# Optimization experiments

Measured on AMD Instinct MI355X. Metric: run time of the kernel, lower is better.

Reference implementation:

```python
import jax, jax.numpy as jnp
import numpy as np

B, L, S, M, N = 128, 3, 256, 256, 20000
NS, A, NL = 4, 5, 2
MAP_RANGE = 10.0
DELTA_VAR = 0.1
EPS = 1e-5


def _ln(x):
    mu = jnp.mean(x, -1, keepdims=True)
    var = jnp.var(x, -1, keepdims=True)
    return (x - mu) / jnp.sqrt(var + EPS)


def _cal_map_last(map_pts, anchor_last):
    # map_pts: [2, N], anchor_last: [B, 1, L] -> [B, M, 2]
    pos = anchor_last[:, 0, 0:2]
    d = map_pts[None, :, :] - pos[:, :, None]                    # [B,2,N]
    th = anchor_last[:, 0, -1]
    c, s = jnp.cos(th), jnp.sin(th)
    rot = jnp.stack([jnp.stack([c, s], -1), jnp.stack([-s, c], -1)], 1)  # [B,2,2]
    m = jnp.einsum('bij,bjn->bin', rot, d)                       # ego-frame points
    dis = jnp.sqrt(jnp.sum(m * m, axis=1, keepdims=True))        # [B,1,N]
    m = jnp.where(dis >= MAP_RANGE, 1e10, m)
    m = jnp.sort(m, axis=-1)                                     # per-coordinate sort (as in torch)
    m = jnp.where(m >= 1e9, 0.0, m)
    m = m[:, :, :M]                                              # torch F.pad negative pad == crop to map_num_max
    return jnp.transpose(m, (0, 2, 1))


def _forward(inp_start_point, map_pts, end_point, delta_limit_mean,
             W_enc_anchor, Wq, Wk, Wv, W_in, W_out, W_map1, W_map2,
             W_ih0, W_ih1, W_hh0, W_hh1, W_m1, W_m2, W_v1, W_v2):
    anchor = inp_start_point
    var_last = jnp.ones_like(anchor) * 0.01  # never updated, as in torch source
    pre_mean, pre_var, views = [], [], []
    scale = 1.0 / np.sqrt(S)                 # MHA 1 head -> head_dim = S
    bsz = anchor.shape[0]
    for step in range(NS):
        dm, dv = [anchor], [var_last]
        vt = [jnp.transpose(_cal_map_last(map_pts, anchor), (0, 2, 1))]
        h = jnp.ones((NL, bsz, S), anchor.dtype)
        c = jnp.ones((NL, bsz, S), anchor.dtype)
        for _ in range(A - 1):
            enc_a = _ln(jnp.concatenate([anchor, anchor - end_point, var_last], -1) @ W_enc_anchor[step].T)  # [B,1,S]
            ml = jax.lax.stop_gradient(_cal_map_last(map_pts, anchor))  # torch.no_grad in encode_last_map
            q = ml @ Wq[step].T
            k = ml @ Wk[step].T
            v = ml @ Wv[step].T
            wq, wk, wv = jnp.split(W_in[step], 3, axis=0)
            q2 = q @ wq.T
            k2 = k @ wk.T
            v2 = v @ wv.T
            attn = jax.nn.softmax(jnp.einsum('bqs,bks->bqk', q2, k2) * scale, axis=-1)
            o = jnp.einsum('bqk,bks->bqs', attn, v2) @ W_out[step].T    # [B,M,S]
            x = jax.nn.relu(jnp.transpose(o, (0, 2, 1)))                # [B,S,M]
            x = jax.nn.relu(x @ W_map1[step].T) @ W_map2[step].T        # [B,S,1]
            enc_m = _ln(jnp.transpose(x, (0, 2, 1)))                    # [B,1,S]
            xl = jnp.concatenate([enc_a, enc_m], -1)[:, 0, :]           # [B,2S], single LSTM timestep
            hs, cs = [], []
            for l, (Wih, Whh) in enumerate(((W_ih0[step], W_hh0[step]), (W_ih1[step], W_hh1[step]))):
                g = xl @ Wih.T + h[l] @ Whh.T
                i_g, f_g, g_g, o_g = jnp.split(g, 4, -1)               # torch gate order i,f,g,o
                cl = jax.nn.sigmoid(f_g) * c[l] + jax.nn.sigmoid(i_g) * jnp.tanh(g_g)
                hl = jax.nn.sigmoid(o_g) * jnp.tanh(cl)
                hs.append(hl)
                cs.append(cl)
                xl = hl
            h, c = jnp.stack(hs), jnp.stack(cs)
            mn = _ln(xl)[:, None, :]                                    # [B,1,S]
            mean = jnp.tanh(jax.nn.relu(jax.nn.relu(mn) @ W_m1[step].T) @ W_m2[step].T) * delta_limit_mean + anchor
            varr = jax.nn.sigmoid(jax.nn.relu(jax.nn.relu(mn) @ W_v1[step].T) @ W_v2[step].T) * DELTA_VAR
            dm.append(mean)
            dv.append(varr)
            anchor = mean
            vt.append(jnp.transpose(_cal_map_last(map_pts, anchor), (0, 2, 1)))
        pre_mean.append(jnp.concatenate(dm, 1)[:, None])    # [B,1,A,L]
        pre_var.append(jnp.concatenate(dv, 1)[:, None])
        views.append(jnp.stack(vt, 1)[:, None])             # [B,1,A,2,M]
    return (jnp.concatenate(pre_mean, 1), jnp.concatenate(pre_var, 1), jnp.concatenate(views, 1))


def setup_inputs() -> dict:
    key = jax.random.key(0)
    ks = jax.random.split(key, 20)

    def w(k, shape, fan):
        return jax.random.normal(k, shape, jnp.float32) / np.sqrt(fan)

    return {
        'inp_start_point': jax.random.normal(ks[0], (B, 1, L), jnp.float32) * 2.0,
        'map_pts': jax.random.uniform(ks[1], (2, N), jnp.float32, -50.0, 50.0),
        'end_point': jnp.array([5.0, 5.0, 0.0], jnp.float32),
        'delta_limit_mean': jnp.array([1.0, 1.0, 0.3], jnp.float32),
        'W_enc_anchor': w(ks[2], (NS, S, 3 * L), 3 * L),
        'Wq': w(ks[3], (NS, S, 2), 2),
        'Wk': w(ks[4], (NS, S, 2), 2),
        'Wv': w(ks[5], (NS, S, 2), 2),
        'W_in': w(ks[6], (NS, 3 * S, S), S),
        'W_out': w(ks[7], (NS, S, S), S),
        'W_map1': w(ks[8], (NS, S, M), M),
        'W_map2': w(ks[9], (NS, 1, S), S),
        'W_ih0': w(ks[10], (NS, 4 * S, 2 * S), 2 * S),
        'W_ih1': w(ks[11], (NS, 4 * S, S), S),
        'W_hh0': w(ks[12], (NS, 4 * S, S), S),
        'W_hh1': w(ks[13], (NS, 4 * S, S), S),
        'W_m1': w(ks[14], (NS, S, S), S),
        'W_m2': w(ks[15], (NS, L, S), S),
        'W_v1': w(ks[16], (NS, S, S), S),
        'W_v2': w(ks[17], (NS, L, S), S),
    }


def reference(inp_start_point, map_pts, end_point, delta_limit_mean,
              W_enc_anchor, Wq, Wk, Wv, W_in, W_out, W_map1, W_map2,
              W_ih0, W_ih1, W_hh0, W_hh1, W_m1, W_m2, W_v1, W_v2):
    return _forward(inp_start_point, map_pts, end_point, delta_limit_mean,
                    W_enc_anchor, Wq, Wk, Wv, W_in, W_out, W_map1, W_map2,
                    W_ih0, W_ih1, W_hh0, W_hh1, W_m1, W_m2, W_v1, W_v2)
```

## Files before the change

### kernel.cpp

```cpp
#include <hip/hip_runtime.h>

#define BB 128
#define NPTS 20000
#define NSTEP 4
#define NITER 4

#define OFF_ANCHOR 0
#define OFF_G      384
#define OFF_AO     400
#define OFF_U      2448
#define OFF_XL     67984
#define OFF_OUT    133520
#define OFF_H      166288
#define OFF_C      231824
#define OFF_GB     297360
#define OFF_RMN    428432
#define OFF_TM     461200
#define OFF_TV     493968

#define OUT_VAR   7680
#define OUT_VIEWS 15360

__device__ __forceinline__ float sigf(float x){ return 1.0f/(1.0f+expf(-x)); }

__device__ __forceinline__ float blockSum256(float v, float* buf){
    for (int off = 32; off > 0; off >>= 1) v += __shfl_down(v, off, 64);
    int tid = threadIdx.x;
    __syncthreads();
    if ((tid & 63) == 0) buf[tid >> 6] = v;
    __syncthreads();
    return (buf[0] + buf[1]) + (buf[2] + buf[3]);
}

__device__ __forceinline__ double blockSum256d(double v, double* buf){
    for (int off = 32; off > 0; off >>= 1) v += __shfl_down(v, off, 64);
    int tid = threadIdx.x;
    __syncthreads();
    if ((tid & 63) == 0) buf[tid >> 6] = v;
    __syncthreads();
    return (buf[0] + buf[1]) + (buf[2] + buf[3]);
}

__global__ __launch_bounds__(256) void k_init(const float* __restrict__ inp, float* __restrict__ ws)
{
    int i = blockIdx.x*256 + threadIdx.x;
    if (i < BB*3) ws[OFF_ANCHOR + i] = inp[i];
}

__global__ __launch_bounds__(256) void k_pre(const float* __restrict__ Wq, const float* __restrict__ Wk,
                                             const float* __restrict__ Wv, const float* __restrict__ Win,
                                             const float* __restrict__ Wout, float* __restrict__ ws)
{
    __shared__ float wql[512], wkl[512], wvl[512];
    __shared__ double avl[512];
    __shared__ double dbuf[4];
    int s = blockIdx.x, t = threadIdx.x;
    wql[t] = Wq[s*512 + t];   wql[256+t] = Wq[s*512 + 256 + t];
    wkl[t] = Wk[s*512 + t];   wkl[256+t] = Wk[s*512 + 256 + t];
    wvl[t] = Wv[s*512 + t];   wvl[256+t] = Wv[s*512 + 256 + t];
    __syncthreads();
    const float* wq = Win + s*196608 + t*256;
    const float* wk = wq + 65536;
    const float* wv = wq + 131072;
    double aq0=0,aq1=0,ak0=0,ak1=0,av0=0,av1=0;
    for (int j = 0; j < 256; j++){
        double a = wq[j], b = wk[j], c = wv[j];
        aq0 += a*(double)wql[j*2]; aq1 += a*(double)wql[j*2+1];
        ak0 += b*(double)wkl[j*2]; ak1 += b*(double)wkl[j*2+1];
        av0 += c*(double)wvl[j*2]; av1 += c*(double)wvl[j*2+1];
    }
    avl[t*2] = av0; avl[t*2+1] = av1;
    double g00 = blockSum256d(aq0*ak0, dbuf);
    double g01 = blockSum256d(aq0*ak1, dbuf);
    double g10 = blockSum256d(aq1*ak0, dbuf);
    double g11 = blockSum256d(aq1*ak1, dbuf);
    if (t == 0){
        ws[OFF_G + s*4+0] = (float)g00; ws[OFF_G + s*4+1] = (float)g01;
        ws[OFF_G + s*4+2] = (float)g10; ws[OFF_G + s*4+3] = (float)g11;
    }
    const float* wo = Wout + s*65536 + t*256;
    double o0 = 0.0, o1 = 0.0;
    for (int j = 0; j < 256; j++){
        double w = wo[j];
        o0 += w*avl[j*2]; o1 += w*avl[j*2+1];
    }
    ws[OFF_AO + s*512 + t*2]   = (float)o0;
    ws[OFF_AO + s*512 + t*2+1] = (float)o1;
}

__global__ __launch_bounds__(256) void k_step_init(float* __restrict__ ws, float* __restrict__ out, int s)
{
    int gid = blockIdx.x*256 + threadIdx.x;
    if (gid < 2*BB*256){ ws[OFF_H + gid] = 1.0f; ws[OFF_C + gid] = 1.0f; }
    if (gid < BB*3){
        int b = gid/3, j = gid - b*3;
        out[((b*NSTEP + s)*5 + 0)*3 + j] = ws[OFF_ANCHOR + gid];
        out[OUT_VAR + ((b*NSTEP + s)*5 + 0)*3 + j] = 0.01f;
    }
}

__global__ __launch_bounds__(256) void k_map(const float* __restrict__ mp, float* __restrict__ ws,
                                             float* __restrict__ out, int s, int t)
{
    __shared__ unsigned int histx[2048], histy[2048];
    __shared__ float vx[1024], vy[1024];
    __shared__ float candx[512], candy[512];
    __shared__ float sortx[256], sorty[256];
    __shared__ int scanb[256];
    __shared__ int shjx, shjy;
    __shared__ unsigned int cnt_in, cntx, cnty;
    int tid = threadIdx.x, b = blockIdx.x;
    float ax = ws[OFF_ANCHOR + b*3 + 0];
    float ay = ws[OFF_ANCHOR + b*3 + 1];
    float th = ws[OFF_ANCHOR + b*3 + 2];
    float cth = cosf(th), sth = sinf(th);
    for (int i = tid; i < 2048; i += 256){ histx[i] = 0u; histy[i] = 0u; }
    if (tid == 0){ cnt_in = 0u; cntx = 0u; cnty = 0u; }
    __syncthreads();
    for (int i = tid; i < NPTS; i += 256){
        float dx = mp[i] - ax, dy = mp[NPTS + i] - ay;
        float rx = cth*dx + sth*dy;
        float ry = cth*dy - sth*dx;
        float d  = sqrtf(rx*rx + ry*ry);
        if (d < 10.0f){
            unsigned p = atomicAdd(&cnt_in, 1u);
            if (p < 1024u){ vx[p] = rx; vy[p] = ry; }
            int bx = (int)((rx + 10.0f) * 102.4f); bx = min(max(bx, 0), 2047);
            int by = (int)((ry + 10.0f) * 102.4f); by = min(max(by, 0), 2047);
            atomicAdd(&histx[bx], 1u); atomicAdd(&histy[by], 1u);
        }
    }
    __syncthreads();
    int total = (int)min(cnt_in, 1024u);
    int K = min(256, total);
    {
        int part = 0;
        for (int k = 0; k < 8; k++) part += (int)histx[tid*8 + k];
        scanb[tid] = part; __syncthreads();
        for (int off = 1; off < 256; off <<= 1){
            int v = (tid >= off) ? scanb[tid - off] : 0; __syncthreads();
            scanb[tid] += v; __syncthreads();
        }
        int incl = scanb[tid], excl = incl - part;
        if (K > 0 && excl < K && incl >= K){
            int c = excl;
            for (int k = 0; k < 8; k++){ c += (int)histx[tid*8+k]; if (c >= K){ shjx = tid*8+k; break; } }
        }
        if (K == 0 && tid == 0) shjx = -1;
        __syncthreads();
    }
    {
        int part = 0;
        for (int k = 0; k < 8; k++) part += (int)histy[tid*8 + k];
        scanb[tid] = part; __syncthreads();
        for (int off = 1; off < 256; off <<= 1){
            int v = (tid >= off) ? scanb[tid - off] : 0; __syncthreads();
            scanb[tid] += v; __syncthreads();
        }
        int incl = scanb[tid], excl = incl - part;
        if (K > 0 && excl < K && incl >= K){
            int c = excl;
            for (int k = 0; k < 8; k++){ c += (int)histy[tid*8+k]; if (c >= K){ shjy = tid*8+k; break; } }
        }
        if (K == 0 && tid == 0) shjy = -1;
        __syncthreads();
    }
    int jx = shjx, jy = shjy;
    for (int i = tid; i < total; i += 256){
        float v = vx[i];
        int bx = (int)((v + 10.0f)*102.4f); bx = min(max(bx,0),2047);
        if (bx <= jx){ unsigned p = atomicAdd(&cntx,1u); if (p < 512u) candx[p] = v; }
        v = vy[i];
        int by = (int)((v + 10.0f)*102.4f); by = min(max(by,0),2047);
        if (by <= jy){ unsigned p = atomicAdd(&cnty,1u); if (p < 512u) candy[p] = v; }
    }
    __syncthreads();
    int cx = (int)min(cntx, 512u), cy = (int)min(cnty, 512u);
    for (int i = tid; i < cx; i += 256){
        float v = candx[i];
        int r = 0;
        for (int j = 0; j < cx; j++){
            float w = candx[j];
            r += (w < v) || (w == v && j < i);
        }
        if (r < 256) sortx[r] = v;
    }
    for (int i = tid; i < cy; i += 256){
        float v = candy[i];
        int r = 0;
        for (int j = 0; j < cy; j++){
            float w = candy[j];
            r += (w < v) || (w == v && j < i);
        }
        if (r < 256) sorty[r] = v;
    }
    __syncthreads();
    int obase = OUT_VIEWS + (((b*NSTEP + s)*5 + t)*2)*256;
    out[obase + tid]       = (tid < K) ? sortx[tid] : 0.0f;
    out[obase + 256 + tid] = (tid < K) ? sorty[tid] : 0.0f;
}

__global__ __launch_bounds__(256) void k_encattn(const float* __restrict__ out, float* __restrict__ ws,
                                                 const float* __restrict__ Wenc, const float* __restrict__ endp,
                                                 int s, int t)
{
    __shared__ float rbuf[4];
    __shared__ float mlx[256], mly[256];
    int b = blockIdx.x, i = threadIdx.x;
    int obase = OUT_VIEWS + (((b*NSTEP + s)*5 + t)*2)*256;
    mlx[i] = out[obase + i];
    mly[i] = out[obase + 256 + i];
    float a0 = ws[OFF_ANCHOR + b*3+0], a1 = ws[OFF_ANCHOR + b*3+1], a2 = ws[OFF_ANCHOR + b*3+2];
    float z[9] = {a0, a1, a2, a0-endp[0], a1-endp[1], a2-endp[2], 0.01f, 0.01f, 0.01f};
    const float* w = Wenc + s*2304 + i*9;
    float acc = 0.f;
    #pragma unroll
    for (int j = 0; j < 9; j++) acc += z[j]*w[j];
    float mu = blockSum256(acc, rbuf) * (1.0f/256.0f);
    float d = acc - mu;
    float var = blockSum256(d*d, rbuf) * (1.0f/256.0f);
    ws[OFF_XL + b*512 + i] = d * rsqrtf(var + 1e-5f);
    float g00 = ws[OFF_G + s*4+0], g01 = ws[OFF_G + s*4+1];
    float g10 = ws[OFF_G + s*4+2], g11 = ws[OFF_G + s*4+3];
    float x = mlx[i], y = mly[i];
    float t0 = g00*x + g10*y;
    float t1 = g01*x + g11*y;
    float mx = -1e30f;
    for (int j = 0; j < 256; j++){
        float l = (t0*mlx[j] + t1*mly[j]) * 0.0625f;
        mx = fmaxf(mx, l);
    }
    float sum = 0.f, ux = 0.f, uy = 0.f;
    for (int j = 0; j < 256; j++){
        float l = (t0*mlx[j] + t1*mly[j]) * 0.0625f;
        float e = expf(l - mx);
        sum += e; ux += e*mlx[j]; uy += e*mly[j];
    }
    float inv = 1.0f/sum;
    ws[OFF_U + b*512 + i*2]   = ux*inv;
    ws[OFF_U + b*512 + i*2+1] = uy*inv;
}

__global__ __launch_bounds__(256) void k_big(float* __restrict__ ws, const float* __restrict__ W1,
                                             const float* __restrict__ W2, int s)
{
    __shared__ __align__(16) float ul[512];
    __shared__ float aol[128];
    __shared__ float w2l[64];
    __shared__ __align__(16) float xt[64*36];
    __shared__ __align__(16) float w1t[64*36];
    __shared__ float red[64*17];
    int sct = blockIdx.x, st = blockIdx.y, b = blockIdx.z;
    int tid = threadIdx.x, tx = tid & 15, ty = tid >> 4;
    {
        float2 uv = *(const float2*)(ws + OFF_U + b*512 + tid*2);
        ul[tid*2] = uv.x; ul[tid*2+1] = uv.y;
        if (tid < 128) aol[tid] = ws[OFF_AO + s*512 + st*128 + tid];
        if (tid < 64)  w2l[tid] = W2[sct*64 + tid];
    }
    __syncthreads();
    float acc[4][4];
    #pragma unroll
    for (int i=0;i<4;i++){
        #pragma unroll
        for (int j=0;j<4;j++) acc[i][j] = 0.f;
    }
    for (int mt = 0; mt < 8; mt++){
        {
            int cl = tid >> 2, f0 = tid & 3;
            const float* g = W1 + (sct*64 + cl)*256 + mt*32 + f0*4;
            float4 v0 = *(const float4*)g;
            float4 v1 = *(const float4*)(g + 16);
            *(float4*)(w1t + cl*36 + f0*4)      = v0;
            *(float4*)(w1t + cl*36 + f0*4 + 16) = v1;
        }
        {
            int r = tid >> 2, mg = tid & 3;
            float A0 = aol[r*2], A1 = aol[r*2+1];
            int m0 = mt*32 + mg*4;
            float4 o0, o1;
            o0.x = fmaxf(A0*ul[(m0+0)*2] + A1*ul[(m0+0)*2+1], 0.f);
            o0.y = fmaxf(A0*ul[(m0+1)*2] + A1*ul[(m0+1)*2+1], 0.f);
            o0.z = fmaxf(A0*ul[(m0+2)*2] + A1*ul[(m0+2)*2+1], 0.f);
            o0.w = fmaxf(A0*ul[(m0+3)*2] + A1*ul[(m0+3)*2+1], 0.f);
            int m1 = mt*32 + (mg+4)*4;
            o1.x = fmaxf(A0*ul[(m1+0)*2] + A1*ul[(m1+0)*2+1], 0.f);
            o1.y = fmaxf(A0*ul[(m1+1)*2] + A1*ul[(m1+1)*2+1], 0.f);
            o1.z = fmaxf(A0*ul[(m1+2)*2] + A1*ul[(m1+2)*2+1], 0.f);
            o1.w = fmaxf(A0*ul[(m1+3)*2] + A1*ul[(m1+3)*2+1], 0.f);
            *(float4*)(xt + r*36 + mg*4)     = o0;
            *(float4*)(xt + r*36 + (mg+4)*4) = o1;
        }
        __syncthreads();
        #pragma unroll
        for (int m4 = 0; m4 < 8; m4++){
            float4 xv[4], wv[4];
            #pragma unroll
            for (int i=0;i<4;i++) xv[i] = *(const float4*)(xt + (ty*4+i)*36 + m4*4);
            #pragma unroll
            for (int j=0;j<4;j++) wv[j] = *(const float4*)(w1t + (tx + 16*j)*36 + m4*4);
            #pragma unroll
            for (int i=0;i<4;i++){
                #pragma unroll
                for (int j=0;j<4;j++){
                    acc[i][j] += xv[i].x*wv[j].x + xv[i].y*wv[j].y + xv[i].z*wv[j].z + xv[i].w*wv[j].w;
                }
            }
        }
        __syncthreads();
    }
    float psum[4];
    #pragma unroll
    for (int i=0;i<4;i++){
        float p = 0.f;
        #pragma unroll
        for (int j=0;j<4;j++) p += fmaxf(acc[i][j], 0.f) * w2l[tx + 16*j];
        psum[i] = p;
        red[(ty*4+i)*17 + tx] = p;
    }
    __syncthreads();
    if (tid < 64){
        float sm = 0.f;
        #pragma unroll
        for (int q=0;q<16;q++) sm += red[tid*17 + q];
        ws[OFF_GB + b*1024 + sct*256 + st*64 + tid] = sm;
    }
}

__global__ __launch_bounds__(256) void k_lnencm(float* __restrict__ ws)
{
    __shared__ float rbuf[4];
    int b = blockIdx.x, t = threadIdx.x;
    const float* p = ws + OFF_GB + b*1024;
    float v = ((p[t] + p[256+t]) + p[512+t]) + p[768+t];
    v = p[t];
    v += p[256+t]; v += p[512+t]; v += p[768+t];
    float mu = blockSum256(v, rbuf) * (1.0f/256.0f);
    float d = v - mu;
    float var = blockSum256(d*d, rbuf) * (1.0f/256.0f);
    ws[OFF_XL + b*512 + 256 + t] = d * rsqrtf(var + 1e-5f);
}

template<int K>
__device__ __forceinline__ void gemm_pass(const float* __restrict__ A, const float* __restrict__ W,
                                          float* As, float* Wsh, float (&acc)[2][4],
                                          int bt, int ot, int tid)
{
    int tx = tid & 15, ty = tid >> 4;
    for (int kt = 0; kt < K/32; kt++){
        {
            int bb = tid >> 3, kk = (tid & 7) * 4;
            float4 v = *(const float4*)(A + (bt*32+bb)*K + kt*32 + kk);
            float* ap = As + bb*33 + kk;
            ap[0]=v.x; ap[1]=v.y; ap[2]=v.z; ap[3]=v.w;
        }
        {
            int oo = tid >> 2, kk = (tid & 3) * 8;
            const float* g = W + (ot*64+oo)*K + kt*32 + kk;
            float4 v0 = *(const float4*)g;
            float4 v1 = *(const float4*)(g + 4);
            float* wp = Wsh + oo*33 + kk;
            wp[0]=v0.x; wp[1]=v0.y; wp[2]=v0.z; wp[3]=v0.w;
            wp[4]=v1.x; wp[5]=v1.y; wp[6]=v1.z; wp[7]=v1.w;
        }
        __syncthreads();
        #pragma unroll
        for (int kk = 0; kk < 32; kk++){
            float a0 = As[(ty*2)*33 + kk], a1 = As[(ty*2+1)*33 + kk];
            float w0 = Wsh[(tx*4)*33+kk],   w1 = Wsh[(tx*4+1)*33+kk];
            float w2 = Wsh[(tx*4+2)*33+kk], w3 = Wsh[(tx*4+3)*33+kk];
            acc[0][0] += a0*w0; acc[0][1] += a0*w1; acc[0][2] += a0*w2; acc[0][3] += a0*w3;
            acc[1][0] += a1*w0; acc[1][1] += a1*w1; acc[1][2] += a1*w2; acc[1][3] += a1*w3;
        }
        __syncthreads();
    }
}

template<int K1, int K2, int RELU>
__global__ __launch_bounds__(256) void k_gemm(const float* __restrict__ A1, const float* __restrict__ W1,
                                              const float* __restrict__ A2, const float* __restrict__ W2,
                                              float* __restrict__ C, int Osz)
{
    __shared__ float As[32*33];
    __shared__ float Wsh[64*33];
    int tid = threadIdx.x, tx = tid & 15, ty = tid >> 4;
    int ot = blockIdx.x, bt = blockIdx.y;
    float acc[2][4];
    #pragma unroll
    for (int i=0;i<2;i++){
        #pragma unroll
        for (int j=0;j<4;j++) acc[i][j]=0.f;
    }
    gemm_pass<K1>(A1, W1, As, Wsh, acc, bt, ot, tid);
    if constexpr (K2 > 0){
        gemm_pass<K2>(A2, W2, As, Wsh, acc, bt, ot, tid);
    }
    #pragma unroll
    for (int i=0;i<2;i++){
        float4 v;
        v.x = acc[i][0]; v.y = acc[i][1]; v.z = acc[i][2]; v.w = acc[i][3];
        if (RELU){ v.x=fmaxf(v.x,0.f); v.y=fmaxf(v.y,0.f); v.z=fmaxf(v.z,0.f); v.w=fmaxf(v.w,0.f); }
        *(float4*)(C + (bt*32+ty*2+i)*Osz + ot*64 + tx*4) = v;
    }
}

__global__ __launch_bounds__(256) void k_heads2(const float* __restrict__ A, const float* __restrict__ Wm1,
                                                const float* __restrict__ Wv1, float* __restrict__ ws)
{
    __shared__ float As[32*33];
    __shared__ float Wsh[64*33];
    int tid = threadIdx.x, tx = tid & 15, ty = tid >> 4;
    int bx = blockIdx.x, bt = blockIdx.y;
    int ot = bx & 3;
    const float* W = (bx < 4) ? Wm1 : Wv1;
    float* C = ws + ((bx < 4) ? OFF_TM : OFF_TV);
    float acc[2][4];
    #pragma unroll
    for (int i=0;i<2;i++){
        #pragma unroll
        for (int j=0;j<4;j++) acc[i][j]=0.f;
    }
    gemm_pass<256>(A, W, As, Wsh, acc, bt, ot, tid);
    #pragma unroll
    for (int i=0;i<2;i++){
        float4 v;
        v.x = fmaxf(acc[i][0],0.f); v.y = fmaxf(acc[i][1],0.f);
        v.z = fmaxf(acc[i][2],0.f); v.w = fmaxf(acc[i][3],0.f);
        *(float4*)(C + (bt*32+ty*2+i)*256 + ot*64 + tx*4) = v;
    }
}

__global__ __launch_bounds__(256) void k_gates(float* __restrict__ ws, int l)
{
    int b = blockIdx.x, t = threadIdx.x;
    const float* g = ws + OFF_GB + b*1024;
    float ig = g[t], fg = g[256+t], gg = g[512+t], og = g[768+t];
    int idx = l*BB*256 + b*256 + t;
    float cold = ws[OFF_C + idx];
    float cl = sigf(fg)*cold + sigf(ig)*tanhf(gg);
    float hl = sigf(og)*tanhf(cl);
    ws[OFF_C + idx] = cl;
    ws[OFF_H + idx] = hl;
}

__global__ __launch_bounds__(256) void k_mn(float* __restrict__ ws)
{
    __shared__ float rbuf[4];
    int b = blockIdx.x, t = threadIdx.x;
    const float* g = ws + OFF_GB + b*1024;
    float ig = g[t], fg = g[256+t], gg = g[512+t], og = g[768+t];
    int idx = BB*256 + b*256 + t;
    float cold = ws[OFF_C + idx];
    float cl = sigf(fg)*cold + sigf(ig)*tanhf(gg);
    float hl = sigf(og)*tanhf(cl);
    ws[OFF_C + idx] = cl;
    ws[OFF_H + idx] = hl;
    float mu = blockSum256(hl, rbuf) * (1.0f/256.0f);
    float d = hl - mu;
    float var = blockSum256(d*d, rbuf) * (1.0f/256.0f);
    ws[OFF_RMN + b*256 + t] = fmaxf(d * rsqrtf(var + 1e-5f), 0.0f);
}

__global__ __launch_bounds__(256) void k_head(const float* __restrict__ Wm2, const float* __restrict__ Wv2,
                                              const float* __restrict__ dlm, float* __restrict__ ws,
                                              float* __restrict__ out, int s, int t)
{
    int b = blockIdx.x, tid = threadIdx.x;
    int w = tid >> 6, lane = tid & 63;
    #pragma unroll
    for (int p = 0; p < 2; p++){
        int oi = p*4 + w;
        if (oi < 6){
            int j = (oi < 3) ? oi : oi - 3;
            const float* tb = ws + ((oi < 3) ? OFF_TM : OFF_TV) + b*256;
            const float* wr = ((oi < 3) ? Wm2 : Wv2) + j*256;
            float pa = 0.f;
            #pragma unroll
            for (int q = 0; q < 4; q++) pa += tb[lane + 64*q] * wr[lane + 64*q];
            for (int off = 32; off > 0; off >>= 1) pa += __shfl_down(pa, off, 64);
            if (lane == 0){
                if (oi < 3){
                    float mv = tanhf(pa) * dlm[j] + ws[OFF_ANCHOR + b*3 + j];
                    out[((b*NSTEP + s)*5 + (t+1))*3 + j] = mv;
                    ws[OFF_ANCHOR + b*3 + j] = mv;
                } else {
                    out[OUT_VAR + ((b*NSTEP + s)*5 + (t+1))*3 + j] = sigf(pa)*0.1f;
                }
            }
        }
    }
}

extern "C" void kernel_launch(void* const* d_in, const int* in_sizes, int n_in,
                              void* d_out, int out_size, void* d_ws, size_t ws_size,
                              hipStream_t stream)
{
    (void)in_sizes; (void)n_in; (void)out_size; (void)ws_size;
    const float* inp  = (const float*)d_in[0];
    const float* mp   = (const float*)d_in[1];
    const float* endp = (const float*)d_in[2];
    const float* dlm  = (const float*)d_in[3];
    const float* Wenc = (const float*)d_in[4];
    const float* Wq   = (const float*)d_in[5];
    const float* Wk   = (const float*)d_in[6];
    const float* Wv   = (const float*)d_in[7];
    const float* Win  = (const float*)d_in[8];
    const float* Wout = (const float*)d_in[9];
    const float* Wmap1= (const float*)d_in[10];
    const float* Wmap2= (const float*)d_in[11];
    const float* Wih0 = (const float*)d_in[12];
    const float* Wih1 = (const float*)d_in[13];
    const float* Whh0 = (const float*)d_in[14];
    const float* Whh1 = (const float*)d_in[15];
    const float* Wm1  = (const float*)d_in[16];
    const float* Wm2  = (const float*)d_in[17];
    const float* Wv1  = (const float*)d_in[18];
    const float* Wv2  = (const float*)d_in[19];
    float* out = (float*)d_out;
    float* ws  = (float*)d_ws;

    k_init<<<2, 256, 0, stream>>>(inp, ws);
    k_pre<<<NSTEP, 256, 0, stream>>>(Wq, Wk, Wv, Win, Wout, ws);
    for (int s = 0; s < NSTEP; s++){
        k_step_init<<<256, 256, 0, stream>>>(ws, out, s);
        for (int t = 0; t < NITER; t++){
            k_map<<<BB, 256, 0, stream>>>(mp, ws, out, s, t);
            k_encattn<<<BB, 256, 0, stream>>>(out, ws, Wenc, endp, s, t);
            k_big<<<dim3(4, 4, BB), 256, 0, stream>>>(ws, Wmap1 + s*65536, Wmap2 + s*256, s);
            k_lnencm<<<BB, 256, 0, stream>>>(ws);
            k_gemm<512,256,0><<<dim3(16,4), 256, 0, stream>>>(ws+OFF_XL, Wih0 + s*524288,
                                                              ws+OFF_H,  Whh0 + s*262144,
                                                              ws+OFF_GB, 1024);
            k_gates<<<BB, 256, 0, stream>>>(ws, 0);
            k_gemm<256,256,0><<<dim3(16,4), 256, 0, stream>>>(ws+OFF_H,          Wih1 + s*262144,
                                                              ws+OFF_H + BB*256, Whh1 + s*262144,
                                                              ws+OFF_GB, 1024);
            k_mn<<<BB, 256, 0, stream>>>(ws);
            k_heads2<<<dim3(8,4), 256, 0, stream>>>(ws+OFF_RMN, Wm1 + s*65536, Wv1 + s*65536, ws);
            k_head<<<BB, 256, 0, stream>>>(Wm2 + s*768, Wv2 + s*768, dlm, ws, out, s, t);
        }
        k_map<<<BB, 256, 0, stream>>>(mp, ws, out, s, 4);
    }
}
```

Measured before the change: 4.492 ms.

## Fuse LSTM, gate and head kernels into per-batch megakernel; merge map and encoder

Merges the map-sort kernel with the encoder/attention kernel, and folds the per-step init and the trailing map pass into it. Replaces the two tiled LSTM GEMMs, gate kernels, layernorm and both head kernels with one per-batch-row kernel that streams the weights through LDS as matrix-vector products. The goal is to cut most of the per-iteration kernel launches and the workspace round trips. The cost is that each of the 128 blocks now re-reads every LSTM and head weight with no reuse across batch rows, and only 128 blocks run. The selection histogram also shrinks from 2048 to 256 bins and the candidate buffer from 512 to 448 entries, which raises the chance of candidate overflow and makes the rank sort larger.

```diff
diff --git a/kernel.cpp b/kernel.cpp
--- a/kernel.cpp
+++ b/kernel.cpp
@@ -10,13 +10,9 @@
 #define OFF_AO     400
 #define OFF_U      2448
 #define OFF_XL     67984
-#define OFF_OUT    133520
 #define OFF_H      166288
 #define OFF_C      231824
 #define OFF_GB     297360
-#define OFF_RMN    428432
-#define OFF_TM     461200
-#define OFF_TV     493968
 
 #define OUT_VAR   7680
 #define OUT_VIEWS 15360
@@ -88,33 +84,24 @@
     ws[OFF_AO + s*512 + t*2+1] = (float)o1;
 }
 
-__global__ __launch_bounds__(256) void k_step_init(float* __restrict__ ws, float* __restrict__ out, int s)
+__global__ __launch_bounds__(256) void k_mapenc(const float* __restrict__ mp, float* __restrict__ ws,
+                                                float* __restrict__ out, const float* __restrict__ Wenc,
+                                                const float* __restrict__ endp, int s, int t, int wprev)
 {
-    int gid = blockIdx.x*256 + threadIdx.x;
-    if (gid < 2*BB*256){ ws[OFF_H + gid] = 1.0f; ws[OFF_C + gid] = 1.0f; }
-    if (gid < BB*3){
-        int b = gid/3, j = gid - b*3;
-        out[((b*NSTEP + s)*5 + 0)*3 + j] = ws[OFF_ANCHOR + gid];
-        out[OUT_VAR + ((b*NSTEP + s)*5 + 0)*3 + j] = 0.01f;
-    }
-}
-
-__global__ __launch_bounds__(256) void k_map(const float* __restrict__ mp, float* __restrict__ ws,
-                                             float* __restrict__ out, int s, int t)
-{
-    __shared__ unsigned int histx[2048], histy[2048];
+    __shared__ unsigned int histx[256], histy[256];
     __shared__ float vx[1024], vy[1024];
-    __shared__ float candx[512], candy[512];
-    __shared__ float sortx[256], sorty[256];
-    __shared__ int scanb[256];
+    __shared__ float candx[448], candy[448];
+    __shared__ float mxS[256], myS[256];
+    __shared__ int scanx[256], scany[256];
     __shared__ int shjx, shjy;
     __shared__ unsigned int cnt_in, cntx, cnty;
+    __shared__ float rbuf[4];
     int tid = threadIdx.x, b = blockIdx.x;
     float ax = ws[OFF_ANCHOR + b*3 + 0];
     float ay = ws[OFF_ANCHOR + b*3 + 1];
     float th = ws[OFF_ANCHOR + b*3 + 2];
     float cth = cosf(th), sth = sinf(th);
-    for (int i = tid; i < 2048; i += 256){ histx[i] = 0u; histy[i] = 0u; }
+    histx[tid] = 0u; histy[tid] = 0u;
     if (tid == 0){ cnt_in = 0u; cntx = 0u; cnty = 0u; }
     __syncthreads();
     for (int i = tid; i < NPTS; i += 256){
@@ -125,120 +112,111 @@
         if (d < 10.0f){
             unsigned p = atomicAdd(&cnt_in, 1u);
             if (p < 1024u){ vx[p] = rx; vy[p] = ry; }
-            int bx = (int)((rx + 10.0f) * 102.4f); bx = min(max(bx, 0), 2047);
-            int by = (int)((ry + 10.0f) * 102.4f); by = min(max(by, 0), 2047);
+            int bx = min(max((int)((rx + 10.0f)*12.8f), 0), 255);
+            int by = min(max((int)((ry + 10.0f)*12.8f), 0), 255);
             atomicAdd(&histx[bx], 1u); atomicAdd(&histy[by], 1u);
         }
     }
     __syncthreads();
     int total = (int)min(cnt_in, 1024u);
     int K = min(256, total);
-    {
-        int part = 0;
-        for (int k = 0; k < 8; k++) part += (int)histx[tid*8 + k];
-        scanb[tid] = part; __syncthreads();
-        for (int off = 1; off < 256; off <<= 1){
-            int v = (tid >= off) ? scanb[tid - off] : 0; __syncthreads();
-            scanb[tid] += v; __syncthreads();
-        }
-        int incl = scanb[tid], excl = incl - part;
-        if (K > 0 && excl < K && incl >= K){
-            int c = excl;
-            for (int k = 0; k < 8; k++){ c += (int)histx[tid*8+k]; if (c >= K){ shjx = tid*8+k; break; } }
-        }
-        if (K == 0 && tid == 0) shjx = -1;
+    int px = (int)histx[tid], py = (int)histy[tid];
+    scanx[tid] = px; scany[tid] = py;
+    __syncthreads();
+    for (int off = 1; off < 256; off <<= 1){
+        int vxs = (tid >= off) ? scanx[tid - off] : 0;
+        int vys = (tid >= off) ? scany[tid - off] : 0;
         __syncthreads();
-    }
-    {
-        int part = 0;
-        for (int k = 0; k < 8; k++) part += (int)histy[tid*8 + k];
-        scanb[tid] = part; __syncthreads();
-        for (int off = 1; off < 256; off <<= 1){
-            int v = (tid >= off) ? scanb[tid - off] : 0; __syncthreads();
-            scanb[tid] += v; __syncthreads();
-        }
-        int incl = scanb[tid], excl = incl - part;
-        if (K > 0 && excl < K && incl >= K){
-            int c = excl;
-            for (int k = 0; k < 8; k++){ c += (int)histy[tid*8+k]; if (c >= K){ shjy = tid*8+k; break; } }
-        }
-        if (K == 0 && tid == 0) shjy = -1;
+        scanx[tid] += vxs; scany[tid] += vys;
         __syncthreads();
     }
+    if (K > 0){
+        if (scanx[tid] - px < K && scanx[tid] >= K) shjx = tid;
+        if (scany[tid] - py < K && scany[tid] >= K) shjy = tid;
+    } else if (tid == 0){ shjx = -1; shjy = -1; }
+    __syncthreads();
     int jx = shjx, jy = shjy;
     for (int i = tid; i < total; i += 256){
         float v = vx[i];
-        int bx = (int)((v + 10.0f)*102.4f); bx = min(max(bx,0),2047);
-        if (bx <= jx){ unsigned p = atomicAdd(&cntx,1u); if (p < 512u) candx[p] = v; }
+        int bx = min(max((int)((v + 10.0f)*12.8f), 0), 255);
+        if (bx <= jx){ unsigned p = atomicAdd(&cntx, 1u); if (p < 448u) candx[p] = v; }
         v = vy[i];
-        int by = (int)((v + 10.0f)*102.4f); by = min(max(by,0),2047);
-        if (by <= jy){ unsigned p = atomicAdd(&cnty,1u); if (p < 512u) candy[p] = v; }
-    }
-    __syncthreads();
-    int cx = (int)min(cntx, 512u), cy = (int)min(cnty, 512u);
+        int by = min(max((int)((v + 10.0f)*12.8f), 0), 255);
+        if (by <= jy){ unsigned p = atomicAdd(&cnty, 1u); if (p < 448u) candy[p] = v; }
+    }
+    __syncthreads();
+    int cx = (int)min(cntx, 448u), cy = (int)min(cnty, 448u);
     for (int i = tid; i < cx; i += 256){
         float v = candx[i];
         int r = 0;
-        for (int j = 0; j < cx; j++){
-            float w = candx[j];
-            r += (w < v) || (w == v && j < i);
-        }
-        if (r < 256) sortx[r] = v;
+        for (int j2 = 0; j2 < cx; j2++){
+            float w2 = candx[j2];
+            r += (w2 < v) || (w2 == v && j2 < i);
+        }
+        if (r < 256) mxS[r] = v;
     }
     for (int i = tid; i < cy; i += 256){
         float v = candy[i];
         int r = 0;
-        for (int j = 0; j < cy; j++){
-            float w = candy[j];
-            r += (w < v) || (w == v && j < i);
-        }
-        if (r < 256) sorty[r] = v;
-    }
-    __syncthreads();
+        for (int j2 = 0; j2 < cy; j2++){
+            float w2 = candy[j2];
+            r += (w2 < v) || (w2 == v && j2 < i);
+        }
+        if (r < 256) myS[r] = v;
+    }
+    __syncthreads();
+    float mlx = (tid < K) ? mxS[tid] : 0.0f;
+    float mly = (tid < K) ? myS[tid] : 0.0f;
     int obase = OUT_VIEWS + (((b*NSTEP + s)*5 + t)*2)*256;
-    out[obase + tid]       = (tid < K) ? sortx[tid] : 0.0f;
-    out[obase + 256 + tid] = (tid < K) ? sorty[tid] : 0.0f;
-}
-
-__global__ __launch_bounds__(256) void k_encattn(const float* __restrict__ out, float* __restrict__ ws,
-                                                 const float* __restrict__ Wenc, const float* __restrict__ endp,
-                                                 int s, int t)
-{
-    __shared__ float rbuf[4];
-    __shared__ float mlx[256], mly[256];
-    int b = blockIdx.x, i = threadIdx.x;
-    int obase = OUT_VIEWS + (((b*NSTEP + s)*5 + t)*2)*256;
-    mlx[i] = out[obase + i];
-    mly[i] = out[obase + 256 + i];
-    float a0 = ws[OFF_ANCHOR + b*3+0], a1 = ws[OFF_ANCHOR + b*3+1], a2 = ws[OFF_ANCHOR + b*3+2];
-    float z[9] = {a0, a1, a2, a0-endp[0], a1-endp[1], a2-endp[2], 0.01f, 0.01f, 0.01f};
-    const float* w = Wenc + s*2304 + i*9;
+    out[obase + tid]       = mlx;
+    out[obase + 256 + tid] = mly;
+    if (wprev){
+        int pbase = OUT_VIEWS + (((b*NSTEP + (s-1))*5 + 4)*2)*256;
+        out[pbase + tid]       = mlx;
+        out[pbase + 256 + tid] = mly;
+    }
+    if (t == 4) return;
+    __syncthreads();
+    mxS[tid] = mlx; myS[tid] = mly;
+    float a0 = ax, a1 = ay, a2 = th;
+    float z9[9] = {a0, a1, a2, a0-endp[0], a1-endp[1], a2-endp[2], 0.01f, 0.01f, 0.01f};
+    const float* w = Wenc + s*2304 + tid*9;
     float acc = 0.f;
     #pragma unroll
-    for (int j = 0; j < 9; j++) acc += z[j]*w[j];
+    for (int j2 = 0; j2 < 9; j2++) acc += z9[j2]*w[j2];
     float mu = blockSum256(acc, rbuf) * (1.0f/256.0f);
-    float d = acc - mu;
-    float var = blockSum256(d*d, rbuf) * (1.0f/256.0f);
-    ws[OFF_XL + b*512 + i] = d * rsqrtf(var + 1e-5f);
+    float dd = acc - mu;
+    float var = blockSum256(dd*dd, rbuf) * (1.0f/256.0f);
+    ws[OFF_XL + b*512 + tid] = dd * rsqrtf(var + 1e-5f);
     float g00 = ws[OFF_G + s*4+0], g01 = ws[OFF_G + s*4+1];
     float g10 = ws[OFF_G + s*4+2], g11 = ws[OFF_G + s*4+3];
-    float x = mlx[i], y = mly[i];
-    float t0 = g00*x + g10*y;
-    float t1 = g01*x + g11*y;
-    float mx = -1e30f;
-    for (int j = 0; j < 256; j++){
-        float l = (t0*mlx[j] + t1*mly[j]) * 0.0625f;
-        mx = fmaxf(mx, l);
+    float xq = mxS[tid], yq = myS[tid];
+    float t0 = g00*xq + g10*yq;
+    float t1 = g01*xq + g11*yq;
+    float mxv = -1e30f;
+    for (int j2 = 0; j2 < 256; j2++){
+        float l = (t0*mxS[j2] + t1*myS[j2]) * 0.0625f;
+        mxv = fmaxf(mxv, l);
     }
     float sum = 0.f, ux = 0.f, uy = 0.f;
-    for (int j = 0; j < 256; j++){
-        float l = (t0*mlx[j] + t1*mly[j]) * 0.0625f;
-        float e = expf(l - mx);
-        sum += e; ux += e*mlx[j]; uy += e*mly[j];
+    for (int j2 = 0; j2 < 256; j2++){
+        float l = (t0*mxS[j2] + t1*myS[j2]) * 0.0625f;
+        float e = expf(l - mxv);
+        sum += e; ux += e*mxS[j2]; uy += e*myS[j2];
     }
     float inv = 1.0f/sum;
-    ws[OFF_U + b*512 + i*2]   = ux*inv;
-    ws[OFF_U + b*512 + i*2+1] = uy*inv;
+    ws[OFF_U + b*512 + tid*2]   = ux*inv;
+    ws[OFF_U + b*512 + tid*2+1] = uy*inv;
+    if (t == 0){
+        ws[OFF_H + b*256 + tid] = 1.0f;
+        ws[OFF_H + BB*256 + b*256 + tid] = 1.0f;
+        ws[OFF_C + b*256 + tid] = 1.0f;
+        ws[OFF_C + BB*256 + b*256 + tid] = 1.0f;
+        if (tid < 3){
+            out[((b*NSTEP + s)*5 + 0)*3 + tid] = ws[OFF_ANCHOR + b*3 + tid];
+            out[OUT_VAR + ((b*NSTEP + s)*5 + 0)*3 + tid] = 0.01f;
+        }
+    }
 }
 
 __global__ __launch_bounds__(256) void k_big(float* __restrict__ ws, const float* __restrict__ W1,
@@ -327,164 +305,177 @@
     }
 }
 
-__global__ __launch_bounds__(256) void k_lnencm(float* __restrict__ ws)
+__global__ __launch_bounds__(256) void k_mega(
+    const float* __restrict__ Wih0, const float* __restrict__ Whh0,
+    const float* __restrict__ Wih1, const float* __restrict__ Whh1,
+    const float* __restrict__ Wm1, const float* __restrict__ Wv1,
+    const float* __restrict__ Wm2, const float* __restrict__ Wv2,
+    const float* __restrict__ dlm, float* __restrict__ ws, float* __restrict__ out,
+    int s, int t)
 {
+    __shared__ float xl[512];
+    __shared__ float av[256];
+    __shared__ float h0l[256];
+    __shared__ float rmn[256];
+    __shared__ float tml[256], tvl[256];
+    __shared__ float Wt[256*33];
     __shared__ float rbuf[4];
-    int b = blockIdx.x, t = threadIdx.x;
-    const float* p = ws + OFF_GB + b*1024;
-    float v = ((p[t] + p[256+t]) + p[512+t]) + p[768+t];
-    v = p[t];
-    v += p[256+t]; v += p[512+t]; v += p[768+t];
-    float mu = blockSum256(v, rbuf) * (1.0f/256.0f);
-    float d = v - mu;
-    float var = blockSum256(d*d, rbuf) * (1.0f/256.0f);
-    ws[OFF_XL + b*512 + 256 + t] = d * rsqrtf(var + 1e-5f);
-}
-
-template<int K>
-__device__ __forceinline__ void gemm_pass(const float* __restrict__ A, const float* __restrict__ W,
-                                          float* As, float* Wsh, float (&acc)[2][4],
-                                          int bt, int ot, int tid)
-{
-    int tx = tid & 15, ty = tid >> 4;
-    for (int kt = 0; kt < K/32; kt++){
-        {
-            int bb = tid >> 3, kk = (tid & 7) * 4;
-            float4 v = *(const float4*)(A + (bt*32+bb)*K + kt*32 + kk);
-            float* ap = As + bb*33 + kk;
-            ap[0]=v.x; ap[1]=v.y; ap[2]=v.z; ap[3]=v.w;
-        }
-        {
-            int oo = tid >> 2, kk = (tid & 3) * 8;
-            const float* g = W + (ot*64+oo)*K + kt*32 + kk;
-            float4 v0 = *(const float4*)g;
-            float4 v1 = *(const float4*)(g + 4);
-            float* wp = Wsh + oo*33 + kk;
-            wp[0]=v0.x; wp[1]=v0.y; wp[2]=v0.z; wp[3]=v0.w;
-            wp[4]=v1.x; wp[5]=v1.y; wp[6]=v1.z; wp[7]=v1.w;
-        }
-        __syncthreads();
+    int b = blockIdx.x, tid = threadIdx.x;
+    int rr0 = tid >> 3, c4 = (tid & 7)*4;
+
+    xl[tid] = ws[OFF_XL + b*512 + tid];
+    {
+        const float* p = ws + OFF_GB + b*1024;
+        float v = p[tid];
+        v += p[256+tid]; v += p[512+tid]; v += p[768+tid];
+        float mu = blockSum256(v, rbuf) * (1.0f/256.0f);
+        float d = v - mu;
+        float var = blockSum256(d*d, rbuf) * (1.0f/256.0f);
+        xl[256+tid] = d * rsqrtf(var + 1e-5f);
+    }
+    av[tid] = ws[OFF_H + b*256 + tid];
+    __syncthreads();
+
+    float g0[4];
+    #pragma unroll
+    for (int og = 0; og < 4; og++){
+        float acc = 0.f;
+        for (int kt = 0; kt < 16; kt++){
+            __syncthreads();
+            #pragma unroll
+            for (int r = 0; r < 8; r++){
+                int ro = rr0 + r*32;
+                float4 w4 = *(const float4*)(Wih0 + (og*256 + ro)*512 + kt*32 + c4);
+                *(float4*)(Wt + ro*33 + c4) = w4;
+            }
+            __syncthreads();
+            #pragma unroll
+            for (int k = 0; k < 32; k++)
+                acc = fmaf(xl[kt*32+k], Wt[tid*33+k], acc);
+        }
+        for (int kt = 0; kt < 8; kt++){
+            __syncthreads();
+            #pragma unroll
+            for (int r = 0; r < 8; r++){
+                int ro = rr0 + r*32;
+                float4 w4 = *(const float4*)(Whh0 + (og*256 + ro)*256 + kt*32 + c4);
+                *(float4*)(Wt + ro*33 + c4) = w4;
+            }
+            __syncthreads();
+            #pragma unroll
+            for (int k = 0; k < 32; k++)
+                acc = fmaf(av[kt*32+k], Wt[tid*33+k], acc);
+        }
+        g0[og] = acc;
+    }
+    __syncthreads();
+
+    {
+        float ig = g0[0], fg = g0[1], gg = g0[2], og_ = g0[3];
+        float cold = ws[OFF_C + b*256 + tid];
+        float cl = sigf(fg)*cold + sigf(ig)*tanhf(gg);
+        float hl = sigf(og_)*tanhf(cl);
+        ws[OFF_C + b*256 + tid] = cl;
+        ws[OFF_H + b*256 + tid] = hl;
+        h0l[tid] = hl;
+        av[tid] = ws[OFF_H + BB*256 + b*256 + tid];
+    }
+    __syncthreads();
+
+    float g1[4];
+    #pragma unroll
+    for (int og = 0; og < 4; og++){
+        float acc = 0.f;
+        for (int kt = 0; kt < 8; kt++){
+            __syncthreads();
+            #pragma unroll
+            for (int r = 0; r < 8; r++){
+                int ro = rr0 + r*32;
+                float4 w4 = *(const float4*)(Wih1 + (og*256 + ro)*256 + kt*32 + c4);
+                *(float4*)(Wt + ro*33 + c4) = w4;
+            }
+            __syncthreads();
+            #pragma unroll
+            for (int k = 0; k < 32; k++)
+                acc = fmaf(h0l[kt*32+k], Wt[tid*33+k], acc);
+        }
+        for (int kt = 0; kt < 8; kt++){
+            __syncthreads();
+            #pragma unroll
+            for (int r = 0; r < 8; r++){
+                int ro = rr0 + r*32;
+                float4 w4 = *(const float4*)(Whh1 + (og*256 + ro)*256 + kt*32 + c4);
+                *(float4*)(Wt + ro*33 + c4) = w4;
+            }
+            __syncthreads();
+            #pragma unroll
+            for (int k = 0; k < 32; k++)
+                acc = fmaf(av[kt*32+k], Wt[tid*33+k], acc);
+        }
+        g1[og] = acc;
+    }
+    __syncthreads();
+
+    {
+        float ig = g1[0], fg = g1[1], gg = g1[2], og_ = g1[3];
+        float cold = ws[OFF_C + BB*256 + b*256 + tid];
+        float cl = sigf(fg)*cold + sigf(ig)*tanhf(gg);
+        float hl = sigf(og_)*tanhf(cl);
+        ws[OFF_C + BB*256 + b*256 + tid] = cl;
+        ws[OFF_H + BB*256 + b*256 + tid] = hl;
+        float mu = blockSum256(hl, rbuf) * (1.0f/256.0f);
+        float d = hl - mu;
+        float var = blockSum256(d*d, rbuf) * (1.0f/256.0f);
+        rmn[tid] = fmaxf(d * rsqrtf(var + 1e-5f), 0.0f);
+    }
+    __syncthreads();
+
+    float ta[2];
+    #pragma unroll
+    for (int og = 0; og < 2; og++){
+        const float* Wh = og ? Wv1 : Wm1;
+        float acc = 0.f;
+        for (int kt = 0; kt < 8; kt++){
+            __syncthreads();
+            #pragma unroll
+            for (int r = 0; r < 8; r++){
+                int ro = rr0 + r*32;
+                float4 w4 = *(const float4*)(Wh + ro*256 + kt*32 + c4);
+                *(float4*)(Wt + ro*33 + c4) = w4;
+            }
+            __syncthreads();
+            #pragma unroll
+            for (int k = 0; k < 32; k++)
+                acc = fmaf(rmn[kt*32+k], Wt[tid*33+k], acc);
+        }
+        ta[og] = acc;
+    }
+    __syncthreads();
+    tml[tid] = fmaxf(ta[0], 0.f);
+    tvl[tid] = fmaxf(ta[1], 0.f);
+    __syncthreads();
+
+    {
+        int w = tid >> 6, lane = tid & 63;
         #pragma unroll
-        for (int kk = 0; kk < 32; kk++){
-            float a0 = As[(ty*2)*33 + kk], a1 = As[(ty*2+1)*33 + kk];
-            float w0 = Wsh[(tx*4)*33+kk],   w1 = Wsh[(tx*4+1)*33+kk];
-            float w2 = Wsh[(tx*4+2)*33+kk], w3 = Wsh[(tx*4+3)*33+kk];
-            acc[0][0] += a0*w0; acc[0][1] += a0*w1; acc[0][2] += a0*w2; acc[0][3] += a0*w3;
-            acc[1][0] += a1*w0; acc[1][1] += a1*w1; acc[1][2] += a1*w2; acc[1][3] += a1*w3;
-        }
-        __syncthreads();
-    }
-}
-
-template<int K1, int K2, int RELU>
-__global__ __launch_bounds__(256) void k_gemm(const float* __restrict__ A1, const float* __restrict__ W1,
-                                              const float* __restrict__ A2, const float* __restrict__ W2,
-                                              float* __restrict__ C, int Osz)
-{
-    __shared__ float As[32*33];
-    __shared__ float Wsh[64*33];
-    int tid = threadIdx.x, tx = tid & 15, ty = tid >> 4;
-    int ot = blockIdx.x, bt = blockIdx.y;
-    float acc[2][4];
-    #pragma unroll
-    for (int i=0;i<2;i++){
-        #pragma unroll
-        for (int j=0;j<4;j++) acc[i][j]=0.f;
-    }
-    gemm_pass<K1>(A1, W1, As, Wsh, acc, bt, ot, tid);
-    if constexpr (K2 > 0){
-        gemm_pass<K2>(A2, W2, As, Wsh, acc, bt, ot, tid);
-    }
-    #pragma unroll
-    for (int i=0;i<2;i++){
-        float4 v;
-        v.x = acc[i][0]; v.y = acc[i][1]; v.z = acc[i][2]; v.w = acc[i][3];
-        if (RELU){ v.x=fmaxf(v.x,0.f); v.y=fmaxf(v.y,0.f); v.z=fmaxf(v.z,0.f); v.w=fmaxf(v.w,0.f); }
-        *(float4*)(C + (bt*32+ty*2+i)*Osz + ot*64 + tx*4) = v;
-    }
-}
-
-__global__ __launch_bounds__(256) void k_heads2(const float* __restrict__ A, const float* __restrict__ Wm1,
-                                                const float* __restrict__ Wv1, float* __restrict__ ws)
-{
-    __shared__ float As[32*33];
-    __shared__ float Wsh[64*33];
-    int tid = threadIdx.x, tx = tid & 15, ty = tid >> 4;
-    int bx = blockIdx.x, bt = blockIdx.y;
-    int ot = bx & 3;
-    const float* W = (bx < 4) ? Wm1 : Wv1;
-    float* C = ws + ((bx < 4) ? OFF_TM : OFF_TV);
-    float acc[2][4];
-    #pragma unroll
-    for (int i=0;i<2;i++){
-        #pragma unroll
-        for (int j=0;j<4;j++) acc[i][j]=0.f;
-    }
-    gemm_pass<256>(A, W, As, Wsh, acc, bt, ot, tid);
-    #pragma unroll
-    for (int i=0;i<2;i++){
-        float4 v;
-        v.x = fmaxf(acc[i][0],0.f); v.y = fmaxf(acc[i][1],0.f);
-        v.z = fmaxf(acc[i][2],0.f); v.w = fmaxf(acc[i][3],0.f);
-        *(float4*)(C + (bt*32+ty*2+i)*256 + ot*64 + tx*4) = v;
-    }
-}
-
-__global__ __launch_bounds__(256) void k_gates(float* __restrict__ ws, int l)
-{
-    int b = blockIdx.x, t = threadIdx.x;
-    const float* g = ws + OFF_GB + b*1024;
-    float ig = g[t], fg = g[256+t], gg = g[512+t], og = g[768+t];
-    int idx = l*BB*256 + b*256 + t;
-    float cold = ws[OFF_C + idx];
-    float cl = sigf(fg)*cold + sigf(ig)*tanhf(gg);
-    float hl = sigf(og)*tanhf(cl);
-    ws[OFF_C + idx] = cl;
-    ws[OFF_H + idx] = hl;
-}
-
-__global__ __launch_bounds__(256) void k_mn(float* __restrict__ ws)
-{
-    __shared__ float rbuf[4];
-    int b = blockIdx.x, t = threadIdx.x;
-    const float* g = ws + OFF_GB + b*1024;
-    float ig = g[t], fg = g[256+t], gg = g[512+t], og = g[768+t];
-    int idx = BB*256 + b*256 + t;
-    float cold = ws[OFF_C + idx];
-    float cl = sigf(fg)*cold + sigf(ig)*tanhf(gg);
-    float hl = sigf(og)*tanhf(cl);
-    ws[OFF_C + idx] = cl;
-    ws[OFF_H + idx] = hl;
-    float mu = blockSum256(hl, rbuf) * (1.0f/256.0f);
-    float d = hl - mu;
-    float var = blockSum256(d*d, rbuf) * (1.0f/256.0f);
-    ws[OFF_RMN + b*256 + t] = fmaxf(d * rsqrtf(var + 1e-5f), 0.0f);
-}
-
-__global__ __launch_bounds__(256) void k_head(const float* __restrict__ Wm2, const float* __restrict__ Wv2,
-                                              const float* __restrict__ dlm, float* __restrict__ ws,
-                                              float* __restrict__ out, int s, int t)
-{
-    int b = blockIdx.x, tid = threadIdx.x;
-    int w = tid >> 6, lane = tid & 63;
-    #pragma unroll
-    for (int p = 0; p < 2; p++){
-        int oi = p*4 + w;
-        if (oi < 6){
-            int j = (oi < 3) ? oi : oi - 3;
-            const float* tb = ws + ((oi < 3) ? OFF_TM : OFF_TV) + b*256;
-            const float* wr = ((oi < 3) ? Wm2 : Wv2) + j*256;
-            float pa = 0.f;
-            #pragma unroll
-            for (int q = 0; q < 4; q++) pa += tb[lane + 64*q] * wr[lane + 64*q];
-            for (int off = 32; off > 0; off >>= 1) pa += __shfl_down(pa, off, 64);
-            if (lane == 0){
-                if (oi < 3){
-                    float mv = tanhf(pa) * dlm[j] + ws[OFF_ANCHOR + b*3 + j];
-                    out[((b*NSTEP + s)*5 + (t+1))*3 + j] = mv;
-                    ws[OFF_ANCHOR + b*3 + j] = mv;
-                } else {
-                    out[OUT_VAR + ((b*NSTEP + s)*5 + (t+1))*3 + j] = sigf(pa)*0.1f;
+        for (int pp = 0; pp < 2; pp++){
+            int oi = pp*4 + w;
+            if (oi < 6){
+                int j = (oi < 3) ? oi : oi - 3;
+                const float* tb = (oi < 3) ? tml : tvl;
+                const float* wr = ((oi < 3) ? Wm2 : Wv2) + j*256;
+                float pa = 0.f;
+                #pragma unroll
+                for (int q = 0; q < 4; q++) pa += tb[lane + 64*q] * wr[lane + 64*q];
+                for (int off = 32; off > 0; off >>= 1) pa += __shfl_down(pa, off, 64);
+                if (lane == 0){
+                    if (oi < 3){
+                        float mv = tanhf(pa) * dlm[j] + ws[OFF_ANCHOR + b*3 + j];
+                        out[((b*NSTEP + s)*5 + (t+1))*3 + j] = mv;
+                        ws[OFF_ANCHOR + b*3 + j] = mv;
+                    } else {
+                        out[OUT_VAR + ((b*NSTEP + s)*5 + (t+1))*3 + j] = sigf(pa)*0.1f;
+                    }
                 }
             }
         }
@@ -522,23 +513,16 @@
     k_init<<<2, 256, 0, stream>>>(inp, ws);
     k_pre<<<NSTEP, 256, 0, stream>>>(Wq, Wk, Wv, Win, Wout, ws);
     for (int s = 0; s < NSTEP; s++){
-        k_step_init<<<256, 256, 0, stream>>>(ws, out, s);
         for (int t = 0; t < NITER; t++){
-            k_map<<<BB, 256, 0, stream>>>(mp, ws, out, s, t);
-            k_encattn<<<BB, 256, 0, stream>>>(out, ws, Wenc, endp, s, t);
+            k_mapenc<<<BB, 256, 0, stream>>>(mp, ws, out, Wenc, endp, s, t,
+                                             (t == 0 && s > 0) ? 1 : 0);
             k_big<<<dim3(4, 4, BB), 256, 0, stream>>>(ws, Wmap1 + s*65536, Wmap2 + s*256, s);
-            k_lnencm<<<BB, 256, 0, stream>>>(ws);
-            k_gemm<512,256,0><<<dim3(16,4), 256, 0, stream>>>(ws+OFF_XL, Wih0 + s*524288,
-                                                              ws+OFF_H,  Whh0 + s*262144,
-                                                              ws+OFF_GB, 1024);
-            k_gates<<<BB, 256, 0, stream>>>(ws, 0);
-            k_gemm<256,256,0><<<dim3(16,4), 256, 0, stream>>>(ws+OFF_H,          Wih1 + s*262144,
-                                                              ws+OFF_H + BB*256, Whh1 + s*262144,
-                                                              ws+OFF_GB, 1024);
-            k_mn<<<BB, 256, 0, stream>>>(ws);
-            k_heads2<<<dim3(8,4), 256, 0, stream>>>(ws+OFF_RMN, Wm1 + s*65536, Wv1 + s*65536, ws);
-            k_head<<<BB, 256, 0, stream>>>(Wm2 + s*768, Wv2 + s*768, dlm, ws, out, s, t);
-        }
-        k_map<<<BB, 256, 0, stream>>>(mp, ws, out, s, 4);
-    }
-}
+            k_mega<<<BB, 256, 0, stream>>>(Wih0 + s*524288, Whh0 + s*262144,
+                                           Wih1 + s*262144, Whh1 + s*262144,
+                                           Wm1 + s*65536,  Wv1 + s*65536,
+                                           Wm2 + s*768,    Wv2 + s*768,
+                                           dlm, ws, out, s, t);
+        }
+    }
+    k_mapenc<<<BB, 256, 0, stream>>>(mp, ws, out, Wenc, endp, 3, 4, 0);
+}
```

Result: slower. 6.897 ms (+53.6%).
